# Optimization experiments

Measured on AMD Instinct MI355X. Metric: run time of the kernel, lower is better.

Reference implementation:

```python
import jax, jax.numpy as jnp
import numpy as np
from jax import lax

N_KERNELS = 11
N_GRAMS = 3
EMB = 300
CONV_OUT = 128
B, QLEN, DLEN = 128, 30, 256


def _kernel_mus(n):
    mus = [1.0]
    bin_size = 2.0 / (n - 1)
    mus.append(1 - bin_size / 2)
    for i in range(1, n - 1):
        mus.append(mus[i] - bin_size)
    return mus


def _kernel_sigmas(n):
    bin_size = 2.0 / (n - 1)
    return [0.001] + [0.5 * bin_size] * (n - 1)


MU = jnp.asarray(np.array(_kernel_mus(N_KERNELS), dtype=np.float32))      # [K]
SIGMA = jnp.asarray(np.array(_kernel_sigmas(N_KERNELS), dtype=np.float32))  # [K]


def setup_inputs() -> dict:
    key = jax.random.key(0)
    ks = jax.random.split(key, 10)
    inp = {
        "query_embeddings": jax.random.normal(ks[0], (B, QLEN, EMB), jnp.float32),
        "document_embeddings": jax.random.normal(ks[1], (B, DLEN, EMB), jnp.float32),
        "query_pad_oov_mask": jnp.ones((B, QLEN), jnp.float32),
        "document_pad_oov_mask": jnp.ones((B, DLEN), jnp.float32),
    }
    # conv weights for n-gram sizes 1..3: [out_ch, in_ch, ksize]
    for i in range(1, N_GRAMS + 1):
        inp[f"conv_w{i}"] = jax.random.normal(ks[1 + i], (CONV_OUT, EMB, i), jnp.float32) * 0.05
        inp[f"conv_b{i}"] = jnp.zeros((CONV_OUT,), jnp.float32)
    inp["dense_w"] = jax.random.uniform(ks[9], (1, N_KERNELS * N_GRAMS * N_GRAMS), jnp.float32,
                                        minval=-0.014, maxval=0.014)
    return inp


def _conv_ngram(x, w, b):
    # x: [B, L, E]; w: [C, E, k]; right-pad by k-1 so output length == L (ConstantPad1d((0,k-1)))
    k = w.shape[-1]
    y = lax.conv_general_dilated(x.transpose(0, 2, 1), w, (1,), [(0, k - 1)],
                                 dimension_numbers=("NCH", "OIH", "NCH"))
    return jax.nn.relu(y + b[None, :, None]).transpose(0, 2, 1)  # [B, L, C]


def _kernel_pool(q, d, qd_mask, q_mask):
    # cosine matrix (AllenNLP CosineMatrixAttention: normalize with +1e-13 eps)
    qn = q / (jnp.linalg.norm(q, axis=-1, keepdims=True) + 1e-13)
    dn = d / (jnp.linalg.norm(d, axis=-1, keepdims=True) + 1e-13)
    cos = jnp.einsum("bqe,bde->bqd", qn, dn) * qd_mask  # [B, Q, D]
    # RBF soft-histogram kernels: [B, Q, D, K]
    k = jnp.exp(-(cos[..., None] - MU) ** 2 / (2.0 * SIGMA ** 2)) * qd_mask[..., None]
    per_kernel_query = k.sum(axis=2)  # [B, Q, K]
    log_pk = jnp.log(jnp.clip(per_kernel_query, 1e-10, None)) * 0.01
    return (log_pk * q_mask[..., None]).sum(axis=1)  # [B, K]


def reference(query_embeddings, document_embeddings, query_pad_oov_mask, document_pad_oov_mask,
              conv_w1, conv_b1, conv_w2, conv_b2, conv_w3, conv_b3, dense_w):
    qd_mask = query_pad_oov_mask[:, :, None] * document_pad_oov_mask[:, None, :]  # [B, Q, D]
    conv_params = [(conv_w1, conv_b1), (conv_w2, conv_b2), (conv_w3, conv_b3)]
    q_res = [_conv_ngram(query_embeddings, w, b) for w, b in conv_params]
    d_res = [_conv_ngram(document_embeddings, w, b) for w, b in conv_params]
    matched = [_kernel_pool(q_res[i], d_res[t], qd_mask, query_pad_oov_mask)
               for i in range(N_GRAMS) for t in range(N_GRAMS)]
    all_grams = jnp.concatenate(matched, axis=1)  # [B, K*9]
    return jnp.squeeze(all_grams @ dense_w.T, axis=1)  # [B]
```

## Files before the change

### kernel.cpp

```cpp
#include <hip/hip_runtime.h>
#include <math.h>


typedef __bf16 bf16x8 __attribute__((ext_vector_type(8)));
typedef float f32x4 __attribute__((ext_vector_type(4)));

#if __has_builtin(__builtin_amdgcn_exp2f)
#define EXP2F(x) __builtin_amdgcn_exp2f(x)
#else
#define EXP2F(x) exp2f(x)
#endif

#define AS_STRIDE 344

static __device__ __forceinline__ unsigned short f2bf(float f) {
  union { float f; unsigned int u; } v; v.f = f;
  unsigned int r = v.u + 0x7FFFu + ((v.u >> 16) & 1u);
  return (unsigned short)(r >> 16);
}

__global__ __launch_bounds__(256) void prep(
    const float* __restrict__ w1, const float* __restrict__ w2,
    const float* __restrict__ w3,
    const float* __restrict__ qemb, const float* __restrict__ demb,
    unsigned short* __restrict__ wt2,
    unsigned short* __restrict__ qx, unsigned short* __restrict__ dx,
    float* __restrict__ out) {
  const int bid = blockIdx.x;
  const int t = threadIdx.x;
  if (bid < 960) {
    int idx = bid * 256 + t;
    if (idx >= 245760) return;
    int jj   = idx & 7;
    int lane = (idx >> 3) & 63;
    int ec   = (idx >> 9) % 10;
    int cb   = (idx / 5120) & 7;
    int p    = idx / 40960;
    const float* w; int k, jt;
    if (p == 0)      { w = w1; k = 1; jt = 0; }
    else if (p <= 2) { w = w2; k = 2; jt = p - 1; }
    else             { w = w3; k = 3; jt = p - 3; }
    int c = cb * 16 + (lane & 15);
    int e = ec * 32 + (lane >> 4) * 8 + jj;
    float v = (e < 300) ? w[(c * 300 + e) * k + jt] : 0.0f;
    wt2[idx] = f2bf(v);
  } else if (bid < 6720) {
    int idx = (bid - 960) * 256 + t;
    if (idx >= 1474560) return;
    int c8   = idx % 40;
    int ridx = idx / 40;
    const float* src; unsigned short* dst; int valid;
    if (ridx < 4096) {
      int b = ridx >> 5, r = ridx & 31;
      valid = (r < 30);
      src = qemb + ((size_t)b * 30 + r) * 300;
      dst = qx + (size_t)ridx * 320;
    } else {
      int rd = ridx - 4096;
      valid = 1;
      src = demb + (size_t)rd * 300;
      dst = dx + (size_t)rd * 320;
    }
    int e = c8 * 8;
    float4 a = make_float4(0.f, 0.f, 0.f, 0.f);
    float4 c = make_float4(0.f, 0.f, 0.f, 0.f);
    if (valid && e < 300)     a = *reinterpret_cast<const float4*>(src + e);
    if (valid && e + 4 < 300) c = *reinterpret_cast<const float4*>(src + e + 4);
    uint4 o;
    o.x = (unsigned int)f2bf(a.x) | ((unsigned int)f2bf(a.y) << 16);
    o.y = (unsigned int)f2bf(a.z) | ((unsigned int)f2bf(a.w) << 16);
    o.z = (unsigned int)f2bf(c.x) | ((unsigned int)f2bf(c.y) << 16);
    o.w = (unsigned int)f2bf(c.z) | ((unsigned int)f2bf(c.w) << 16);
    *reinterpret_cast<uint4*>(dst + e) = o;
  } else {
    if (t < 128) out[t] = 0.0f;
  }
}

template<int NI>
__device__ __forceinline__ void conv_body(
    unsigned short* As, float* psq,
    const unsigned short* __restrict__ xs, int L, int Lpad, int l0, int b,
    const unsigned short* __restrict__ wt2,
    const float* __restrict__ b1, const float* __restrict__ b2,
    const float* __restrict__ b3,
    unsigned short* __restrict__ out) {
  constexpr int ROWS = NI * 16 + 2;
  constexpr int NR = NI * 16;
  const int t = threadIdx.x;
  const int w = __builtin_amdgcn_readfirstlane(t >> 6);
  const int lane = t & 63;
  const int quad = lane >> 4, lrow = lane & 15;

  for (int idx = t; idx < ROWS * 40; idx += 512) {
    int r = idx / 40, c = idx % 40;
    int l = l0 + r;
    uint4 v = make_uint4(0u, 0u, 0u, 0u);
    if (l < Lpad) v = *reinterpret_cast<const uint4*>(xs + (size_t)l * 320 + c * 8);
    *reinterpret_cast<uint4*>(&As[r * AS_STRIDE + c * 8]) = v;
  }
  __syncthreads();

  f32x4 acc[NI][3];
  #pragma unroll
  for (int ni = 0; ni < NI; ++ni)
    #pragma unroll
    for (int g = 0; g < 3; ++g) acc[ni][g] = (f32x4){0.f, 0.f, 0.f, 0.f};

  const unsigned short* wl = wt2 + (size_t)lane * 8;

  #pragma unroll 2
  for (int ec = 0; ec < 10; ++ec) {
    #pragma unroll
    for (int j = 0; j < 3; ++j) {
      bf16x8 xf[NI];
      #pragma unroll
      for (int ni = 0; ni < NI; ++ni)
        xf[ni] = *reinterpret_cast<const bf16x8*>(
            &As[(ni * 16 + lrow + j) * AS_STRIDE + ec * 32 + quad * 8]);
      #pragma unroll
      for (int g = j; g < 3; ++g) {
        const int pst = (g * (g + 1)) >> 1;
        bf16x8 wf = *reinterpret_cast<const bf16x8*>(
            wl + ((((pst + j) * 8 + w) * 10 + ec) << 9));
        #pragma unroll
        for (int ni = 0; ni < NI; ++ni)
          acc[ni][g] = __builtin_amdgcn_mfma_f32_16x16x32_bf16(
              wf, xf[ni], acc[ni][g], 0, 0, 0);
      }
    }
  }

  const float* biases[3] = {b1, b2, b3};
  float4 bv[3];
  #pragma unroll
  for (int g = 0; g < 3; ++g)
    bv[g] = *reinterpret_cast<const float4*>(biases[g] + w * 16 + quad * 4);

  #pragma unroll
  for (int ni = 0; ni < NI; ++ni) {
    #pragma unroll
    for (int g = 0; g < 3; ++g) {
      float p = 0.f;
      #pragma unroll
      for (int r = 0; r < 4; ++r) {
        float y = fmaxf(acc[ni][g][r] + bv[g][r], 0.f);
        p += y * y;
      }
      p += __shfl_xor(p, 16);
      p += __shfl_xor(p, 32);
      if (lane < 16) psq[(w * 3 + g) * NR + ni * 16 + lrow] = p;
    }
  }
  __syncthreads();

  #pragma unroll
  for (int ni = 0; ni < NI; ++ni) {
    int row = ni * 16 + lrow;
    int l = l0 + row;
    if (l < L) {
      #pragma unroll
      for (int g = 0; g < 3; ++g) {
        float ssq = 0.f;
        #pragma unroll
        for (int wv = 0; wv < 8; ++wv) ssq += psq[(wv * 3 + g) * NR + row];
        float inv = 1.0f / (sqrtf(ssq) + 1e-13f);
        unsigned int pk[2];
        #pragma unroll
        for (int h = 0; h < 2; ++h) {
          float y0 = fmaxf(acc[ni][g][2 * h + 0] + bv[g][2 * h + 0], 0.f) * inv;
          float y1 = fmaxf(acc[ni][g][2 * h + 1] + bv[g][2 * h + 1], 0.f) * inv;
          pk[h] = (unsigned int)f2bf(y0) | ((unsigned int)f2bf(y1) << 16);
        }
        unsigned short* op = out + ((size_t)(g * 128 + b) * L + l) * 128 +
                             w * 16 + quad * 4;
        *reinterpret_cast<uint2*>(op) = make_uint2(pk[0], pk[1]);
      }
    }
  }
}

__global__ __launch_bounds__(512, 4) void conv_all(
    const unsigned short* __restrict__ qx, const unsigned short* __restrict__ dx,
    const unsigned short* __restrict__ wt2,
    const float* __restrict__ b1, const float* __restrict__ b2,
    const float* __restrict__ b3,
    unsigned short* __restrict__ qn, unsigned short* __restrict__ dn) {
  __shared__ unsigned short As[66 * AS_STRIDE];
  __shared__ float psq[8 * 3 * 64];
  const int bi = blockIdx.x;
  if (bi < 512)
    conv_body<4>(As, psq, dx + (size_t)(bi >> 2) * 256 * 320, 256, 256,
                 (bi & 3) * 64, bi >> 2, wt2, b1, b2, b3, dn);
  else
    conv_body<2>(As, psq, qx + (size_t)(bi - 512) * 32 * 320, 30, 32,
                 0, bi - 512, wt2, b1, b2, b3, qn);
}

__global__ __launch_bounds__(512) void pool_final(
    const unsigned short* __restrict__ qn, const unsigned short* __restrict__ dn,
    const float* __restrict__ qmask, const float* __restrict__ dmask,
    const float* __restrict__ dw, float* __restrict__ out) {
  const float MU[11] = {1.0f, 0.9f, 0.7f, 0.5f, 0.3f, 0.1f,
                        -0.1f, -0.3f, -0.5f, -0.7f, -0.9f};
  const float NEGC[11] = {-721347.52f, -72.134752f, -72.134752f, -72.134752f,
                          -72.134752f, -72.134752f, -72.134752f, -72.134752f,
                          -72.134752f, -72.134752f, -72.134752f};
  __shared__ float pf[3 * 30 * 11];
  __shared__ float part[8];

  const int tg = blockIdx.x;
  const int b  = blockIdx.y;
  const int t  = threadIdx.x;
  const int wv = t >> 6, lane = t & 63;
  const int quad = lane >> 4, l15 = lane & 15;
  const int d0 = wv * 32;

  for (int idx = t; idx < 990; idx += 512) pf[idx] = 0.f;

  const unsigned short* dslab = dn + (size_t)(tg * 128 + b) * 256 * 128;

  bf16x8 aD[2][4];
  #pragma unroll
  for (int mi = 0; mi < 2; ++mi)
    #pragma unroll
    for (int kt = 0; kt < 4; ++kt)
      aD[mi][kt] = *reinterpret_cast<const bf16x8*>(
          dslab + (size_t)(d0 + mi * 16 + l15) * 128 + kt * 32 + quad * 8);

  float dmv[2][4];
  #pragma unroll
  for (int mi = 0; mi < 2; ++mi)
    #pragma unroll
    for (int r = 0; r < 4; ++r)
      dmv[mi][r] = dmask[b * 256 + d0 + mi * 16 + quad * 4 + r];

  float qmv[2];
  qmv[0] = qmask[b * 30 + l15];
  qmv[1] = (16 + l15 < 30) ? qmask[b * 30 + 16 + l15] : 0.0f;

  __syncthreads();

  #pragma unroll 1
  for (int ig = 0; ig < 3; ++ig) {
    const unsigned short* qslab = qn + (size_t)(ig * 128 + b) * 30 * 128;

    bf16x8 bQ[2][4];
    #pragma unroll
    for (int ni = 0; ni < 2; ++ni)
      #pragma unroll
      for (int kt = 0; kt < 4; ++kt)
        bQ[ni][kt] = *reinterpret_cast<const bf16x8*>(
            qslab + (size_t)(ni * 16 + l15) * 128 + kt * 32 + quad * 8);

    f32x4 acc[2][2];
    #pragma unroll
    for (int mi = 0; mi < 2; ++mi)
      #pragma unroll
      for (int ni = 0; ni < 2; ++ni) acc[mi][ni] = (f32x4){0.f, 0.f, 0.f, 0.f};

    #pragma unroll
    for (int kt = 0; kt < 4; ++kt)
      #pragma unroll
      for (int mi = 0; mi < 2; ++mi)
        #pragma unroll
        for (int ni = 0; ni < 2; ++ni)
          acc[mi][ni] = __builtin_amdgcn_mfma_f32_16x16x32_bf16(
              aD[mi][kt], bQ[ni][kt], acc[mi][ni], 0, 0, 0);

    float feat[2][11];
    #pragma unroll
    for (int ni = 0; ni < 2; ++ni)
      #pragma unroll
      for (int kk = 0; kk < 11; ++kk) feat[ni][kk] = 0.0f;

    #pragma unroll
    for (int mi = 0; mi < 2; ++mi) {
      #pragma unroll
      for (int r = 0; r < 4; ++r) {
        #pragma unroll
        for (int ni = 0; ni < 2; ++ni) {
          float m  = qmv[ni] * dmv[mi][r];
          float cm = acc[mi][ni][r] * m;
          #pragma unroll
          for (int kk = 0; kk < 11; ++kk) {
            float d2 = cm - MU[kk];
            feat[ni][kk] += EXP2F(d2 * d2 * NEGC[kk]) * m;
          }
        }
      }
    }

    #pragma unroll
    for (int ni = 0; ni < 2; ++ni)
      #pragma unroll
      for (int kk = 0; kk < 11; ++kk) {
        float v = feat[ni][kk];
        v += __shfl_xor(v, 16);
        v += __shfl_xor(v, 32);
        feat[ni][kk] = v;
      }

    if (quad == 0) {
      #pragma unroll
      for (int ni = 0; ni < 2; ++ni) {
        int q = ni * 16 + l15;
        if (q < 30) {
          #pragma unroll
          for (int kk = 0; kk < 11; ++kk)
            atomicAdd(&pf[(ig * 30 + q) * 11 + kk], feat[ni][kk]);
        }
      }
    }
  }
  __syncthreads();

  float s = 0.f;
  for (int idx = t; idx < 990; idx += 512) {
    int ig = idx / 330;
    int rem = idx % 330;
    int q  = rem / 11;
    int kk = rem % 11;
    float v = pf[idx];
    s += __logf(fmaxf(v, 1e-10f)) * 0.01f * qmask[b * 30 + q] *
         dw[(ig * 3 + tg) * 11 + kk];
  }
  s += __shfl_xor(s, 1);  s += __shfl_xor(s, 2);  s += __shfl_xor(s, 4);
  s += __shfl_xor(s, 8);  s += __shfl_xor(s, 16); s += __shfl_xor(s, 32);
  if (lane == 0) part[wv] = s;
  __syncthreads();
  if (t == 0) {
    float tot = 0.f;
    #pragma unroll
    for (int i = 0; i < 8; ++i) tot += part[i];
    atomicAdd(&out[b], tot);
  }
}

extern "C" void kernel_launch(void* const* d_in, const int* in_sizes, int n_in,
                              void* d_out, int out_size, void* d_ws, size_t ws_size,
                              hipStream_t stream) {
  const float* qemb  = (const float*)d_in[0];
  const float* demb  = (const float*)d_in[1];
  const float* qmask = (const float*)d_in[2];
  const float* dmask = (const float*)d_in[3];
  const float* w1 = (const float*)d_in[4];
  const float* b1 = (const float*)d_in[5];
  const float* w2 = (const float*)d_in[6];
  const float* b2 = (const float*)d_in[7];
  const float* w3 = (const float*)d_in[8];
  const float* b3 = (const float*)d_in[9];
  const float* dw = (const float*)d_in[10];

  unsigned short* ws  = (unsigned short*)d_ws;
  unsigned short* wt2 = ws;
  unsigned short* qx  = ws + 245760;
  unsigned short* dx  = ws + 1556480;
  unsigned short* qn  = ws + 12042240;
  unsigned short* dn  = ws + 13516800;
  float* out = (float*)d_out;

  prep<<<6721, 256, 0, stream>>>(w1, w2, w3, qemb, demb, wt2, qx, dx, out);
  conv_all<<<640, 512, 0, stream>>>(qx, dx, wt2, b1, b2, b3, qn, dn);
  pool_final<<<dim3(3, 128), 512, 0, stream>>>(qn, dn, qmask, dmask, dw, out);
}
```

Baseline: 182.7 us.

## Fuse bf16 input conversion into conv and pooling into last-arriving conv block

Conv blocks now read fp32 embeddings directly and convert them to bf16 while staging into shared memory, so the prep pass no longer writes bf16 copies of the inputs. The separate pooling kernel is merged into the conv kernel. A per-batch atomic counter lets the fifth (last) block for each batch run the kernel-pooling for all three document n-grams and write the output directly. This removes a kernel launch and the global round-trip for the converted inputs. In exchange, pooling for each batch runs serially in one block over three n-gram groups rather than across three parallel blocks, and correctness depends on threadfence ordering.

```diff
diff --git a/kernel.cpp b/kernel.cpp
--- a/kernel.cpp
+++ b/kernel.cpp
@@ -22,10 +22,7 @@
 __global__ __launch_bounds__(256) void prep(
     const float* __restrict__ w1, const float* __restrict__ w2,
     const float* __restrict__ w3,
-    const float* __restrict__ qemb, const float* __restrict__ demb,
-    unsigned short* __restrict__ wt2,
-    unsigned short* __restrict__ qx, unsigned short* __restrict__ dx,
-    float* __restrict__ out) {
+    unsigned short* __restrict__ wt2, int* __restrict__ cnt) {
   const int bid = blockIdx.x;
   const int t = threadIdx.x;
   if (bid < 960) {
@@ -44,43 +41,15 @@
     int e = ec * 32 + (lane >> 4) * 8 + jj;
     float v = (e < 300) ? w[(c * 300 + e) * k + jt] : 0.0f;
     wt2[idx] = f2bf(v);
-  } else if (bid < 6720) {
-    int idx = (bid - 960) * 256 + t;
-    if (idx >= 1474560) return;
-    int c8   = idx % 40;
-    int ridx = idx / 40;
-    const float* src; unsigned short* dst; int valid;
-    if (ridx < 4096) {
-      int b = ridx >> 5, r = ridx & 31;
-      valid = (r < 30);
-      src = qemb + ((size_t)b * 30 + r) * 300;
-      dst = qx + (size_t)ridx * 320;
-    } else {
-      int rd = ridx - 4096;
-      valid = 1;
-      src = demb + (size_t)rd * 300;
-      dst = dx + (size_t)rd * 320;
-    }
-    int e = c8 * 8;
-    float4 a = make_float4(0.f, 0.f, 0.f, 0.f);
-    float4 c = make_float4(0.f, 0.f, 0.f, 0.f);
-    if (valid && e < 300)     a = *reinterpret_cast<const float4*>(src + e);
-    if (valid && e + 4 < 300) c = *reinterpret_cast<const float4*>(src + e + 4);
-    uint4 o;
-    o.x = (unsigned int)f2bf(a.x) | ((unsigned int)f2bf(a.y) << 16);
-    o.y = (unsigned int)f2bf(a.z) | ((unsigned int)f2bf(a.w) << 16);
-    o.z = (unsigned int)f2bf(c.x) | ((unsigned int)f2bf(c.y) << 16);
-    o.w = (unsigned int)f2bf(c.z) | ((unsigned int)f2bf(c.w) << 16);
-    *reinterpret_cast<uint4*>(dst + e) = o;
   } else {
-    if (t < 128) out[t] = 0.0f;
+    if (t < 128) cnt[t] = 0;
   }
 }
 
 template<int NI>
 __device__ __forceinline__ void conv_body(
     unsigned short* As, float* psq,
-    const unsigned short* __restrict__ xs, int L, int Lpad, int l0, int b,
+    const float* __restrict__ xb, int L, int l0, int b,
     const unsigned short* __restrict__ wt2,
     const float* __restrict__ b1, const float* __restrict__ b2,
     const float* __restrict__ b3,
@@ -92,12 +61,15 @@
   const int lane = t & 63;
   const int quad = lane >> 4, lrow = lane & 15;
 
-  for (int idx = t; idx < ROWS * 40; idx += 512) {
-    int r = idx / 40, c = idx % 40;
+  for (int idx = t; idx < ROWS * 80; idx += 512) {
+    int r = idx / 80, e4 = idx % 80;
+    int e = e4 * 4;
     int l = l0 + r;
-    uint4 v = make_uint4(0u, 0u, 0u, 0u);
-    if (l < Lpad) v = *reinterpret_cast<const uint4*>(xs + (size_t)l * 320 + c * 8);
-    *reinterpret_cast<uint4*>(&As[r * AS_STRIDE + c * 8]) = v;
+    float4 v = make_float4(0.f, 0.f, 0.f, 0.f);
+    if (l < L && e < 300) v = *reinterpret_cast<const float4*>(xb + (size_t)l * 300 + e);
+    unsigned int lo = (unsigned int)f2bf(v.x) | ((unsigned int)f2bf(v.y) << 16);
+    unsigned int hi = (unsigned int)f2bf(v.z) | ((unsigned int)f2bf(v.w) << 16);
+    *reinterpret_cast<uint2*>(&As[r * AS_STRIDE + e]) = make_uint2(lo, hi);
   }
   __syncthreads();
 
@@ -180,54 +152,53 @@
   }
 }
 
-__global__ __launch_bounds__(512, 4) void conv_all(
-    const unsigned short* __restrict__ qx, const unsigned short* __restrict__ dx,
+__global__ __launch_bounds__(512, 4) void conv_pool(
+    const float* __restrict__ qemb, const float* __restrict__ demb,
+    const float* __restrict__ qmask, const float* __restrict__ dmask,
+    const float* __restrict__ b1, const float* __restrict__ b2,
+    const float* __restrict__ b3, const float* __restrict__ dw,
     const unsigned short* __restrict__ wt2,
-    const float* __restrict__ b1, const float* __restrict__ b2,
-    const float* __restrict__ b3,
-    unsigned short* __restrict__ qn, unsigned short* __restrict__ dn) {
+    unsigned short* __restrict__ qn, unsigned short* __restrict__ dn,
+    int* __restrict__ cnt, float* __restrict__ out) {
   __shared__ unsigned short As[66 * AS_STRIDE];
   __shared__ float psq[8 * 3 * 64];
+  __shared__ int lastFlag;
+
   const int bi = blockIdx.x;
-  if (bi < 512)
-    conv_body<4>(As, psq, dx + (size_t)(bi >> 2) * 256 * 320, 256, 256,
-                 (bi & 3) * 64, bi >> 2, wt2, b1, b2, b3, dn);
-  else
-    conv_body<2>(As, psq, qx + (size_t)(bi - 512) * 32 * 320, 30, 32,
-                 0, bi - 512, wt2, b1, b2, b3, qn);
-}
-
-__global__ __launch_bounds__(512) void pool_final(
-    const unsigned short* __restrict__ qn, const unsigned short* __restrict__ dn,
-    const float* __restrict__ qmask, const float* __restrict__ dmask,
-    const float* __restrict__ dw, float* __restrict__ out) {
+  const int t = threadIdx.x;
+  int b;
+  if (bi < 512) {
+    b = bi >> 2;
+    conv_body<4>(As, psq, demb + (size_t)b * 256 * 300, 256,
+                 (bi & 3) * 64, b, wt2, b1, b2, b3, dn);
+  } else {
+    b = bi - 512;
+    conv_body<2>(As, psq, qemb + (size_t)b * 30 * 300, 30,
+                 0, b, wt2, b1, b2, b3, qn);
+  }
+
+  __syncthreads();
+  if (t == 0) {
+    __threadfence();
+    lastFlag = (atomicAdd(&cnt[b], 1) == 4);
+  }
+  __syncthreads();
+  if (!lastFlag) return;
+
+  __threadfence();
+
   const float MU[11] = {1.0f, 0.9f, 0.7f, 0.5f, 0.3f, 0.1f,
                         -0.1f, -0.3f, -0.5f, -0.7f, -0.9f};
   const float NEGC[11] = {-721347.52f, -72.134752f, -72.134752f, -72.134752f,
                           -72.134752f, -72.134752f, -72.134752f, -72.134752f,
                           -72.134752f, -72.134752f, -72.134752f};
-  __shared__ float pf[3 * 30 * 11];
-  __shared__ float part[8];
-
-  const int tg = blockIdx.x;
-  const int b  = blockIdx.y;
-  const int t  = threadIdx.x;
+  float* pf = psq;
+  float* part = psq + 1024;
+
   const int wv = t >> 6, lane = t & 63;
   const int quad = lane >> 4, l15 = lane & 15;
   const int d0 = wv * 32;
 
-  for (int idx = t; idx < 990; idx += 512) pf[idx] = 0.f;
-
-  const unsigned short* dslab = dn + (size_t)(tg * 128 + b) * 256 * 128;
-
-  bf16x8 aD[2][4];
-  #pragma unroll
-  for (int mi = 0; mi < 2; ++mi)
-    #pragma unroll
-    for (int kt = 0; kt < 4; ++kt)
-      aD[mi][kt] = *reinterpret_cast<const bf16x8*>(
-          dslab + (size_t)(d0 + mi * 16 + l15) * 128 + kt * 32 + quad * 8);
-
   float dmv[2][4];
   #pragma unroll
   for (int mi = 0; mi < 2; ++mi)
@@ -239,101 +210,118 @@
   qmv[0] = qmask[b * 30 + l15];
   qmv[1] = (16 + l15 < 30) ? qmask[b * 30 + 16 + l15] : 0.0f;
 
-  __syncthreads();
+  float s = 0.f;
 
   #pragma unroll 1
-  for (int ig = 0; ig < 3; ++ig) {
-    const unsigned short* qslab = qn + (size_t)(ig * 128 + b) * 30 * 128;
-
-    bf16x8 bQ[2][4];
-    #pragma unroll
-    for (int ni = 0; ni < 2; ++ni)
+  for (int tg = 0; tg < 3; ++tg) {
+    __syncthreads();
+    for (int idx = t; idx < 990; idx += 512) pf[idx] = 0.f;
+
+    const unsigned short* dslab = dn + (size_t)(tg * 128 + b) * 256 * 128;
+    bf16x8 aD[2][4];
+    #pragma unroll
+    for (int mi = 0; mi < 2; ++mi)
       #pragma unroll
       for (int kt = 0; kt < 4; ++kt)
-        bQ[ni][kt] = *reinterpret_cast<const bf16x8*>(
-            qslab + (size_t)(ni * 16 + l15) * 128 + kt * 32 + quad * 8);
-
-    f32x4 acc[2][2];
-    #pragma unroll
-    for (int mi = 0; mi < 2; ++mi)
-      #pragma unroll
-      for (int ni = 0; ni < 2; ++ni) acc[mi][ni] = (f32x4){0.f, 0.f, 0.f, 0.f};
-
-    #pragma unroll
-    for (int kt = 0; kt < 4; ++kt)
+        aD[mi][kt] = *reinterpret_cast<const bf16x8*>(
+            dslab + (size_t)(d0 + mi * 16 + l15) * 128 + kt * 32 + quad * 8);
+
+    __syncthreads();
+
+    #pragma unroll 1
+    for (int ig = 0; ig < 3; ++ig) {
+      const unsigned short* qslab = qn + (size_t)(ig * 128 + b) * 30 * 128;
+
+      bf16x8 bQ[2][4];
+      #pragma unroll
+      for (int ni = 0; ni < 2; ++ni)
+        #pragma unroll
+        for (int kt = 0; kt < 4; ++kt)
+          bQ[ni][kt] = *reinterpret_cast<const bf16x8*>(
+              qslab + (size_t)(ni * 16 + l15) * 128 + kt * 32 + quad * 8);
+
+      f32x4 acc[2][2];
       #pragma unroll
       for (int mi = 0; mi < 2; ++mi)
         #pragma unroll
-        for (int ni = 0; ni < 2; ++ni)
-          acc[mi][ni] = __builtin_amdgcn_mfma_f32_16x16x32_bf16(
-              aD[mi][kt], bQ[ni][kt], acc[mi][ni], 0, 0, 0);
-
-    float feat[2][11];
-    #pragma unroll
-    for (int ni = 0; ni < 2; ++ni)
-      #pragma unroll
-      for (int kk = 0; kk < 11; ++kk) feat[ni][kk] = 0.0f;
-
-    #pragma unroll
-    for (int mi = 0; mi < 2; ++mi) {
-      #pragma unroll
-      for (int r = 0; r < 4; ++r) {
-        #pragma unroll
-        for (int ni = 0; ni < 2; ++ni) {
-          float m  = qmv[ni] * dmv[mi][r];
-          float cm = acc[mi][ni][r] * m;
+        for (int ni = 0; ni < 2; ++ni) acc[mi][ni] = (f32x4){0.f, 0.f, 0.f, 0.f};
+
+      #pragma unroll
+      for (int kt = 0; kt < 4; ++kt)
+        #pragma unroll
+        for (int mi = 0; mi < 2; ++mi)
           #pragma unroll
-          for (int kk = 0; kk < 11; ++kk) {
-            float d2 = cm - MU[kk];
-            feat[ni][kk] += EXP2F(d2 * d2 * NEGC[kk]) * m;
+          for (int ni = 0; ni < 2; ++ni)
+            acc[mi][ni] = __builtin_amdgcn_mfma_f32_16x16x32_bf16(
+                aD[mi][kt], bQ[ni][kt], acc[mi][ni], 0, 0, 0);
+
+      float feat[2][11];
+      #pragma unroll
+      for (int ni = 0; ni < 2; ++ni)
+        #pragma unroll
+        for (int kk = 0; kk < 11; ++kk) feat[ni][kk] = 0.0f;
+
+      #pragma unroll
+      for (int mi = 0; mi < 2; ++mi) {
+        #pragma unroll
+        for (int r = 0; r < 4; ++r) {
+          #pragma unroll
+          for (int ni = 0; ni < 2; ++ni) {
+            float m  = qmv[ni] * dmv[mi][r];
+            float cm = acc[mi][ni][r] * m;
+            #pragma unroll
+            for (int kk = 0; kk < 11; ++kk) {
+              float d2 = cm - MU[kk];
+              feat[ni][kk] += EXP2F(d2 * d2 * NEGC[kk]) * m;
+            }
           }
         }
       }
-    }
-
-    #pragma unroll
-    for (int ni = 0; ni < 2; ++ni)
-      #pragma unroll
-      for (int kk = 0; kk < 11; ++kk) {
-        float v = feat[ni][kk];
-        v += __shfl_xor(v, 16);
-        v += __shfl_xor(v, 32);
-        feat[ni][kk] = v;
-      }
-
-    if (quad == 0) {
-      #pragma unroll
-      for (int ni = 0; ni < 2; ++ni) {
-        int q = ni * 16 + l15;
-        if (q < 30) {
-          #pragma unroll
-          for (int kk = 0; kk < 11; ++kk)
-            atomicAdd(&pf[(ig * 30 + q) * 11 + kk], feat[ni][kk]);
+
+      #pragma unroll
+      for (int ni = 0; ni < 2; ++ni)
+        #pragma unroll
+        for (int kk = 0; kk < 11; ++kk) {
+          float v = feat[ni][kk];
+          v += __shfl_xor(v, 16);
+          v += __shfl_xor(v, 32);
+          feat[ni][kk] = v;
         }
-      }
-    }
-  }
-  __syncthreads();
-
-  float s = 0.f;
-  for (int idx = t; idx < 990; idx += 512) {
-    int ig = idx / 330;
-    int rem = idx % 330;
-    int q  = rem / 11;
-    int kk = rem % 11;
-    float v = pf[idx];
-    s += __logf(fmaxf(v, 1e-10f)) * 0.01f * qmask[b * 30 + q] *
-         dw[(ig * 3 + tg) * 11 + kk];
-  }
+
+      if (quad == 0) {
+        #pragma unroll
+        for (int ni = 0; ni < 2; ++ni) {
+          int q = ni * 16 + l15;
+          if (q < 30) {
+            #pragma unroll
+            for (int kk = 0; kk < 11; ++kk)
+              atomicAdd(&pf[(ig * 30 + q) * 11 + kk], feat[ni][kk]);
+          }
+        }
+      }
+    }
+    __syncthreads();
+
+    for (int idx = t; idx < 990; idx += 512) {
+      int ig = idx / 330;
+      int rem = idx % 330;
+      int q  = rem / 11;
+      int kk = rem % 11;
+      s += __logf(fmaxf(pf[idx], 1e-10f)) * 0.01f * qmask[b * 30 + q] *
+           dw[(ig * 3 + tg) * 11 + kk];
+    }
+  }
+
   s += __shfl_xor(s, 1);  s += __shfl_xor(s, 2);  s += __shfl_xor(s, 4);
   s += __shfl_xor(s, 8);  s += __shfl_xor(s, 16); s += __shfl_xor(s, 32);
+  __syncthreads();
   if (lane == 0) part[wv] = s;
   __syncthreads();
   if (t == 0) {
     float tot = 0.f;
     #pragma unroll
     for (int i = 0; i < 8; ++i) tot += part[i];
-    atomicAdd(&out[b], tot);
+    out[b] = tot;
   }
 }
 
@@ -354,13 +342,12 @@
 
   unsigned short* ws  = (unsigned short*)d_ws;
   unsigned short* wt2 = ws;
-  unsigned short* qx  = ws + 245760;
-  unsigned short* dx  = ws + 1556480;
-  unsigned short* qn  = ws + 12042240;
-  unsigned short* dn  = ws + 13516800;
+  unsigned short* qn  = ws + 245760;
+  unsigned short* dn  = ws + 1720320;
+  int*            cnt = (int*)(ws + 14303232);
   float* out = (float*)d_out;
 
-  prep<<<6721, 256, 0, stream>>>(w1, w2, w3, qemb, demb, wt2, qx, dx, out);
-  conv_all<<<640, 512, 0, stream>>>(qx, dx, wt2, b1, b2, b3, qn, dn);
-  pool_final<<<dim3(3, 128), 512, 0, stream>>>(qn, dn, qmask, dmask, dw, out);
-}
+  prep<<<961, 256, 0, stream>>>(w1, w2, w3, wt2, cnt);
+  conv_pool<<<640, 512, 0, stream>>>(qemb, demb, qmask, dmask,
+                                     b1, b2, b3, dw, wt2, qn, dn, cnt, out);
+}
```

After: 230.9 us. 26.4% more time.

## Split pooling into per-chunk single-wave blocks with separate final reduction kernel

Applied to the files above, without the earlier changes.

The pooling kernel is restructured from 384 blocks of 8 waves, which used shared-memory atomics, into 3072 single-wave blocks. Each block writes its partial per-query kernel sums to a workspace buffer that reuses the now-dead qx region, and a new final kernel sums the 8 chunks and applies log, mask and dense weights. This drops the output zeroing and global atomics. The RBF exponent is algebraically expanded so each kernel costs one FMA before exp2. The conv kernel reuses As shared memory for psq behind an added barrier and unrolls its loop by 5 instead of 2. The split adds a fourth launch and extra global traffic for the partials.

```diff
diff --git a/kernel.cpp b/kernel.cpp
--- a/kernel.cpp
+++ b/kernel.cpp
@@ -24,8 +24,7 @@
     const float* __restrict__ w3,
     const float* __restrict__ qemb, const float* __restrict__ demb,
     unsigned short* __restrict__ wt2,
-    unsigned short* __restrict__ qx, unsigned short* __restrict__ dx,
-    float* __restrict__ out) {
+    unsigned short* __restrict__ qx, unsigned short* __restrict__ dx) {
   const int bid = blockIdx.x;
   const int t = threadIdx.x;
   if (bid < 960) {
@@ -44,7 +43,7 @@
     int e = ec * 32 + (lane >> 4) * 8 + jj;
     float v = (e < 300) ? w[(c * 300 + e) * k + jt] : 0.0f;
     wt2[idx] = f2bf(v);
-  } else if (bid < 6720) {
+  } else {
     int idx = (bid - 960) * 256 + t;
     if (idx >= 1474560) return;
     int c8   = idx % 40;
@@ -72,14 +71,12 @@
     o.z = (unsigned int)f2bf(c.x) | ((unsigned int)f2bf(c.y) << 16);
     o.w = (unsigned int)f2bf(c.z) | ((unsigned int)f2bf(c.w) << 16);
     *reinterpret_cast<uint4*>(dst + e) = o;
-  } else {
-    if (t < 128) out[t] = 0.0f;
   }
 }
 
 template<int NI>
 __device__ __forceinline__ void conv_body(
-    unsigned short* As, float* psq,
+    unsigned short* As,
     const unsigned short* __restrict__ xs, int L, int Lpad, int l0, int b,
     const unsigned short* __restrict__ wt2,
     const float* __restrict__ b1, const float* __restrict__ b2,
@@ -109,7 +106,7 @@
 
   const unsigned short* wl = wt2 + (size_t)lane * 8;
 
-  #pragma unroll 2
+  #pragma unroll 5
   for (int ec = 0; ec < 10; ++ec) {
     #pragma unroll
     for (int j = 0; j < 3; ++j) {
@@ -130,6 +127,8 @@
       }
     }
   }
+  __syncthreads();
+  float* psq = (float*)As;
 
   const float* biases[3] = {b1, b2, b3};
   float4 bv[3];
@@ -187,36 +186,30 @@
     const float* __restrict__ b3,
     unsigned short* __restrict__ qn, unsigned short* __restrict__ dn) {
   __shared__ unsigned short As[66 * AS_STRIDE];
-  __shared__ float psq[8 * 3 * 64];
   const int bi = blockIdx.x;
   if (bi < 512)
-    conv_body<4>(As, psq, dx + (size_t)(bi >> 2) * 256 * 320, 256, 256,
+    conv_body<4>(As, dx + (size_t)(bi >> 2) * 256 * 320, 256, 256,
                  (bi & 3) * 64, bi >> 2, wt2, b1, b2, b3, dn);
   else
-    conv_body<2>(As, psq, qx + (size_t)(bi - 512) * 32 * 320, 30, 32,
+    conv_body<2>(As, qx + (size_t)(bi - 512) * 32 * 320, 30, 32,
                  0, bi - 512, wt2, b1, b2, b3, qn);
 }
 
-__global__ __launch_bounds__(512) void pool_final(
+__global__ __launch_bounds__(64) void pool_mfma(
     const unsigned short* __restrict__ qn, const unsigned short* __restrict__ dn,
     const float* __restrict__ qmask, const float* __restrict__ dmask,
-    const float* __restrict__ dw, float* __restrict__ out) {
-  const float MU[11] = {1.0f, 0.9f, 0.7f, 0.5f, 0.3f, 0.1f,
-                        -0.1f, -0.3f, -0.5f, -0.7f, -0.9f};
-  const float NEGC[11] = {-721347.52f, -72.134752f, -72.134752f, -72.134752f,
-                          -72.134752f, -72.134752f, -72.134752f, -72.134752f,
-                          -72.134752f, -72.134752f, -72.134752f};
-  __shared__ float pf[3 * 30 * 11];
-  __shared__ float part[8];
-
-  const int tg = blockIdx.x;
-  const int b  = blockIdx.y;
-  const int t  = threadIdx.x;
-  const int wv = t >> 6, lane = t & 63;
-  const int quad = lane >> 4, l15 = lane & 15;
-  const int d0 = wv * 32;
-
-  for (int idx = t; idx < 990; idx += 512) pf[idx] = 0.f;
+    float* __restrict__ pkq8) {
+  const float A2[11] = {2.0f, 1.8f, 1.4f, 1.0f, 0.6f, 0.2f,
+                        -0.2f, -0.6f, -1.0f, -1.4f, -1.8f};
+  const float CC[11] = {-721347.52f, -58.429149f, -35.346028f, -18.033688f,
+                        -6.4921277f, -0.72134752f, -0.72134752f, -6.4921277f,
+                        -18.033688f, -35.346028f, -58.429149f};
+  const int tg    = blockIdx.x >> 3;
+  const int chunk = blockIdx.x & 7;
+  const int b     = blockIdx.y;
+  const int lane  = threadIdx.x;
+  const int quad  = lane >> 4, l15 = lane & 15;
+  const int d0    = chunk * 32;
 
   const unsigned short* dslab = dn + (size_t)(tg * 128 + b) * 256 * 128;
 
@@ -239,8 +232,6 @@
   qmv[0] = qmask[b * 30 + l15];
   qmv[1] = (16 + l15 < 30) ? qmask[b * 30 + 16 + l15] : 0.0f;
 
-  __syncthreads();
-
   #pragma unroll 1
   for (int ig = 0; ig < 3; ++ig) {
     const unsigned short* qslab = qn + (size_t)(ig * 128 + b) * 30 * 128;
@@ -282,10 +273,13 @@
         for (int ni = 0; ni < 2; ++ni) {
           float m  = qmv[ni] * dmv[mi][r];
           float cm = acc[mi][ni][r] * m;
+          float w0 = cm * -721347.52f;
+          float w1 = cm * -72.134752f;
           #pragma unroll
           for (int kk = 0; kk < 11; ++kk) {
-            float d2 = cm - MU[kk];
-            feat[ni][kk] += EXP2F(d2 * d2 * NEGC[kk]) * m;
+            float wk = (kk == 0) ? w0 : w1;
+            float e = EXP2F(fmaf(wk, cm - A2[kk], CC[kk]));
+            feat[ni][kk] += e * m;
           }
         }
       }
@@ -302,39 +296,45 @@
       }
 
     if (quad == 0) {
+      const int pair = ig * 3 + tg;
       #pragma unroll
       for (int ni = 0; ni < 2; ++ni) {
         int q = ni * 16 + l15;
         if (q < 30) {
+          float* p = pkq8 +
+              (((size_t)(chunk * 9 + pair) * 128 + b) * 30 + q) * 11;
           #pragma unroll
-          for (int kk = 0; kk < 11; ++kk)
-            atomicAdd(&pf[(ig * 30 + q) * 11 + kk], feat[ni][kk]);
+          for (int kk = 0; kk < 11; ++kk) p[kk] = feat[ni][kk];
         }
       }
     }
   }
-  __syncthreads();
-
-  float s = 0.f;
-  for (int idx = t; idx < 990; idx += 512) {
-    int ig = idx / 330;
-    int rem = idx % 330;
-    int q  = rem / 11;
-    int kk = rem % 11;
-    float v = pf[idx];
-    s += __logf(fmaxf(v, 1e-10f)) * 0.01f * qmask[b * 30 + q] *
-         dw[(ig * 3 + tg) * 11 + kk];
+}
+
+__global__ __launch_bounds__(256) void final_kernel(
+    const float* __restrict__ pkq8, const float* __restrict__ qmask,
+    const float* __restrict__ dw, float* __restrict__ out) {
+  const int CH = 9 * 128 * 30 * 11;
+  const int b = blockIdx.x;
+  const int t = threadIdx.x;
+  float s = 0.0f;
+  for (int idx = t; idx < 9 * 30 * 11; idx += 256) {
+    int pair = idx / 330;
+    int rem  = idx % 330;
+    int q    = rem / 11;
+    int kk   = rem % 11;
+    size_t base = (((size_t)pair * 128 + b) * 30 + q) * 11 + kk;
+    float v = 0.f;
+    #pragma unroll
+    for (int c = 0; c < 8; ++c) v += pkq8[base + (size_t)c * CH];
+    s += __logf(fmaxf(v, 1e-10f)) * 0.01f * qmask[b * 30 + q] * dw[pair * 11 + kk];
   }
   s += __shfl_xor(s, 1);  s += __shfl_xor(s, 2);  s += __shfl_xor(s, 4);
   s += __shfl_xor(s, 8);  s += __shfl_xor(s, 16); s += __shfl_xor(s, 32);
-  if (lane == 0) part[wv] = s;
+  __shared__ float part[4];
+  if ((t & 63) == 0) part[t >> 6] = s;
   __syncthreads();
-  if (t == 0) {
-    float tot = 0.f;
-    #pragma unroll
-    for (int i = 0; i < 8; ++i) tot += part[i];
-    atomicAdd(&out[b], tot);
-  }
+  if (t == 0) out[b] = part[0] + part[1] + part[2] + part[3];
 }
 
 extern "C" void kernel_launch(void* const* d_in, const int* in_sizes, int n_in,
@@ -358,9 +358,11 @@
   unsigned short* dx  = ws + 1556480;
   unsigned short* qn  = ws + 12042240;
   unsigned short* dn  = ws + 13516800;
+  float*          pkq8 = (float*)(ws + 245760);
   float* out = (float*)d_out;
 
-  prep<<<6721, 256, 0, stream>>>(w1, w2, w3, qemb, demb, wt2, qx, dx, out);
+  prep<<<6720, 256, 0, stream>>>(w1, w2, w3, qemb, demb, wt2, qx, dx);
   conv_all<<<640, 512, 0, stream>>>(qx, dx, wt2, b1, b2, b3, qn, dn);
-  pool_final<<<dim3(3, 128), 512, 0, stream>>>(qn, dn, qmask, dmask, dw, out);
-}
+  pool_mfma<<<dim3(24, 128), 64, 0, stream>>>(qn, dn, qmask, dmask, pkq8);
+  final_kernel<<<128, 256, 0, stream>>>(pkq8, qmask, dw, out);
+}
```

New measurement: 179.3 us. About the same (-1.8%).
